# Optimization experiments

Hardware: AMD Instinct MI355X
Metric: run time of the kernel (lower is better)

The kernel has to match this reference:

```python
import jax, jax.numpy as jnp
import numpy as np

N = 8192
M = 16
F_NODE = 128
HID = 512


def setup_inputs() -> dict:
    key = jax.random.key(0)
    ks = jax.random.split(key, 10)
    node_in_fea = jax.random.normal(ks[0], (N, F_NODE), dtype=jnp.float32)
    edge_fea_idx = jax.random.randint(ks[1], (N, M), 0, N, dtype=jnp.int64)
    s_emb = 1.0 / np.sqrt(F_NODE)
    s_h = 1.0 / np.sqrt(HID)
    W_emb = jax.random.uniform(ks[2], (F_NODE, HID), jnp.float32, -s_emb, s_emb)
    b_emb = jax.random.uniform(ks[3], (HID,), jnp.float32, -s_emb, s_emb)
    W1 = jax.random.uniform(ks[4], (HID, HID), jnp.float32, -s_h, s_h)
    b1 = jax.random.uniform(ks[5], (HID,), jnp.float32, -s_h, s_h)
    W2 = jax.random.uniform(ks[6], (HID, HID), jnp.float32, -s_h, s_h)
    b2 = jax.random.uniform(ks[7], (HID,), jnp.float32, -s_h, s_h)
    W3 = jax.random.uniform(ks[8], (HID, HID), jnp.float32, -s_h, s_h)
    b3 = jax.random.uniform(ks[9], (HID,), jnp.float32, -s_h, s_h)
    return {"node_in_fea": node_in_fea, "edge_fea_idx": edge_fea_idx,
            "W_emb": W_emb, "b_emb": b_emb, "W1": W1, "b1": b1,
            "W2": W2, "b2": b2, "W3": W3, "b3": b3}


def _normalized_adj(edge_fea_idx, n):
    # build dense adjacency: adj[i, j] += 1 for each valid neighbor j of i
    rows = jnp.broadcast_to(jnp.arange(n)[:, None], edge_fea_idx.shape)
    valid = edge_fea_idx >= 0  # -1 marks invalid neighbor
    cols = jnp.where(valid, edge_fea_idx, 0)
    vals = valid.astype(jnp.float32)
    adj = jnp.zeros((n, n), jnp.float32).at[rows.reshape(-1), cols.reshape(-1)].add(vals.reshape(-1))
    # add self-loops, symmetric normalization D^{-1/2} A D^{-1/2}
    adj = adj + jnp.eye(n, dtype=jnp.float32)
    deg = jnp.sum(adj, axis=1)
    d_inv_sqrt = jnp.where(deg > 0, deg ** -0.5, 0.0)
    return adj * d_inv_sqrt[:, None] * d_inv_sqrt[None, :]


def reference(node_in_fea, edge_fea_idx, W_emb, b_emb, W1, b1, W2, b2, W3, b3):
    adj = _normalized_adj(edge_fea_idx, node_in_fea.shape[0])
    x = node_in_fea @ W_emb + b_emb          # (N, HID)
    x = jax.nn.relu((adj @ x) @ W1 + b1)     # gcn1 + relu
    x = jax.nn.relu((adj @ x) @ W2 + b2)     # gcn2 + relu
    x = (adj @ x) @ W3 + b3                  # gcn3 (no relu)
    return x
```

## Files before the change

### kernel.cpp

```cpp
#include <hip/hip_runtime.h>
#include <stdint.h>

#define NN 8192
#define MM 16
#define FN 128
#define HH 512

typedef unsigned short u16;
typedef unsigned int u32;
typedef __bf16 bf16;
typedef __bf16 bf16x8 __attribute__((ext_vector_type(8)));
typedef float f32x4 __attribute__((ext_vector_type(4)));

__device__ __forceinline__ void gld_lds16(const u16* g, u16* l) {
  __builtin_amdgcn_global_load_lds(
      (const __attribute__((address_space(1))) void*)g,
      (__attribute__((address_space(3))) void*)l, 16, 0, 0);
}

__device__ __forceinline__ int probe_f32(const u16* w) {
  int lane = threadIdx.x & 63;
  int e = (w[2 * lane] >> 7) & 0xFF;
  unsigned long long m = __ballot(!(e == 0 || (e >= 90 && e <= 140)));
  return __popcll(m) >= 8;
}
__device__ __forceinline__ int probe_i64(const u32* w) {
  int lane = threadIdx.x & 63;
  unsigned long long m = __ballot(lane < 32 && w[2 * lane + 1] != 0);
  return m == 0;
}

__device__ __forceinline__ void transpose_tile(const void* __restrict__ W,
                                               u16* __restrict__ T, int K,
                                               int tt, int f32in, u16* sm) {
  const int k0 = (tt >> 4) * 32, n0 = (tt & 15) * 32;
  const int tx = threadIdx.x & 31, ty = threadIdx.x >> 5;
#pragma unroll
  for (int r = ty; r < 32; r += 8) {
    size_t src = (size_t)(k0 + r) * HH + n0 + tx;
    bf16 v = f32in ? (bf16)((const float*)W)[src] : ((const bf16*)W)[src];
    sm[r * 33 + tx] = *(u16*)&v;
  }
  __syncthreads();
#pragma unroll
  for (int r = ty; r < 32; r += 8)
    T[(size_t)(n0 + r) * K + k0 + tx] = sm[tx * 33 + r];
}

__global__ __launch_bounds__(256) void prepA_kernel(
    const u16* __restrict__ node, const void* __restrict__ Wemb,
    const void* __restrict__ b0, u16* __restrict__ biasBF,
    u16* __restrict__ TWemb) {
  __shared__ u16 sm[32 * 33];
  const int f32in = probe_f32(node);
  const int bid = blockIdx.x, tid = threadIdx.x;
  if (bid < 2) {
    const int off = bid * 256 + tid;
    bf16 v = f32in ? (bf16)((const float*)b0)[off] : ((const bf16*)b0)[off];
    biasBF[off] = *(u16*)&v;
  } else {
    transpose_tile(Wemb, TWemb, FN, bid - 2, f32in, sm);
  }
}

template <bool RELU>
__device__ __forceinline__ void gemm_tile(const void* __restrict__ A, int K,
                                          int af32, const u16* __restrict__ Bt,
                                          const u16* __restrict__ bias,
                                          int rtile, int ctile, int outf32,
                                          void* __restrict__ C, u16* As,
                                          u16* Bs) {
  const int tid = threadIdx.x;
  const int wave = tid >> 6, lane = tid & 63;
  const int wr = wave >> 1, wc = wave & 1;
  const int quad = lane >> 4, l16 = lane & 15;
  f32x4 acc[2][4] = {};

  int arow[2], agc[2], brow[4], bgc[4];
#pragma unroll
  for (int i = 0; i < 2; ++i) {
    int c = i * 256 + tid;
    arow[i] = c >> 3;
    agc[i] = (c & 7) ^ (arow[i] & 7);
  }
#pragma unroll
  for (int i = 0; i < 4; ++i) {
    int c = i * 256 + tid;
    brow[i] = c >> 3;
    bgc[i] = (c & 7) ^ (brow[i] & 7);
  }
  u16* AsW = As + wave * 512;
  u16* BsW = Bs + wave * 512;

  for (int k0 = 0; k0 < K; k0 += 64) {
    __syncthreads();
    if (af32) {
      const float* Af = (const float*)A;
      bf16x8 v[2];
#pragma unroll
      for (int i = 0; i < 2; ++i) {
        const float* p = &Af[(size_t)(rtile * 64 + arow[i]) * K + k0 + agc[i] * 8];
        f32x4 x0 = *(const f32x4*)p, x1 = *(const f32x4*)(p + 4);
#pragma unroll
        for (int t = 0; t < 4; ++t) {
          v[i][t] = (bf16)x0[t];
          v[i][4 + t] = (bf16)x1[t];
        }
      }
#pragma unroll
      for (int i = 0; i < 2; ++i) *(bf16x8*)&As[(i * 256 + tid) * 8] = v[i];
    } else {
      const u16* Ab = (const u16*)A;
#pragma unroll
      for (int i = 0; i < 2; ++i)
        gld_lds16(&Ab[(size_t)(rtile * 64 + arow[i]) * K + k0 + agc[i] * 8],
                  AsW + i * 2048);
    }
#pragma unroll
    for (int i = 0; i < 4; ++i)
      gld_lds16(&Bt[(size_t)(ctile * 128 + brow[i]) * K + k0 + bgc[i] * 8],
                BsW + i * 2048);
    __syncthreads();
#pragma unroll
    for (int h = 0; h < 2; ++h) {
      bf16x8 af[2], bfr[4];
#pragma unroll
      for (int i = 0; i < 2; ++i) {
        int r = wr * 32 + i * 16 + l16;
        int cc = (h * 4 + quad) ^ (r & 7);
        af[i] = *(const bf16x8*)&As[r * 64 + cc * 8];
      }
#pragma unroll
      for (int j = 0; j < 4; ++j) {
        int n = wc * 64 + j * 16 + l16;
        int cc = (h * 4 + quad) ^ (n & 7);
        bfr[j] = *(const bf16x8*)&Bs[n * 64 + cc * 8];
      }
#pragma unroll
      for (int i = 0; i < 2; ++i)
#pragma unroll
        for (int j = 0; j < 4; ++j)
          acc[i][j] = __builtin_amdgcn_mfma_f32_16x16x32_bf16(af[i], bfr[j],
                                                              acc[i][j], 0, 0, 0);
    }
  }

  const int crow0 = rtile * 64 + wr * 32 + quad * 4;
  const int ccol0 = ctile * 128 + wc * 64 + l16;
#pragma unroll
  for (int j = 0; j < 4; ++j) {
    const int col = ccol0 + j * 16;
    const float bv = (float)(*(const bf16*)&bias[col]);
#pragma unroll
    for (int i = 0; i < 2; ++i)
#pragma unroll
      for (int r = 0; r < 4; ++r) {
        float v = acc[i][j][r] + bv;
        if (RELU) v = fmaxf(v, 0.0f);
        size_t off = (size_t)(crow0 + i * 16 + r) * HH + col;
        if (outf32) {
          ((float*)C)[off] = v;
        } else {
          bf16 o = (bf16)v;
          ((u16*)C)[off] = *(u16*)&o;
        }
      }
  }
}

__global__ __launch_bounds__(256) void emb_plus_kernel(
    const u16* __restrict__ node, const u32* __restrict__ idxw,
    const void* __restrict__ W1, const void* __restrict__ b1,
    const void* __restrict__ W2, const void* __restrict__ b2,
    const void* __restrict__ W3, const void* __restrict__ b3,
    const u16* __restrict__ TWemb, const u16* __restrict__ biasBF,
    float* __restrict__ dis, u16* __restrict__ biasBF_w,
    u16* __restrict__ TW1, u16* __restrict__ TW2, u16* __restrict__ TW3,
    u16* __restrict__ xout) {
  __shared__ __align__(16) u16 As[64 * 64];
  __shared__ __align__(16) u16 Bs[128 * 64];
  const int bid = blockIdx.x, tid = threadIdx.x;
  if (bid < 512) {
    const int af32 = probe_f32(node);
    gemm_tile<false>(node, FN, af32, TWemb, biasBF, bid >> 2, bid & 3, 0, xout,
                     As, Bs);
  } else if (bid < 544) {
    const int i64 = probe_i64(idxw);
    const int* idx = (const int*)idxw;
    const int i = (bid - 512) * 256 + tid;
    int c = 1;
#pragma unroll
    for (int e = 0; e < MM; ++e) c += (idx[(i * MM + e) << i64] >= 0) ? 1 : 0;
    dis[i] = rsqrtf((float)c);
  } else if (bid < 550) {
    const int f32in = probe_f32(node);
    const int id = (bid - 544) * 256 + tid;
    const int q = id >> 9;
    const void* src = q == 0 ? b1 : q == 1 ? b2 : b3;
    const int off = id & (HH - 1);
    bf16 v = f32in ? (bf16)((const float*)src)[off] : ((const bf16*)src)[off];
    biasBF_w[HH + id] = *(u16*)&v;
  } else {
    const int f32in = probe_f32(node);
    const int t = bid - 550;
    const int q = t >> 8, tt = t & 255;
    const void* W = q == 0 ? W1 : q == 1 ? W2 : W3;
    u16* T = q == 0 ? TW1 : q == 1 ? TW2 : TW3;
    transpose_tile(W, T, HH, tt, f32in, As);
  }
}

template <bool RELU, bool FINAL>
__global__ __launch_bounds__(256) void gemm_main(const u16* __restrict__ A,
                                                 const u16* __restrict__ Bt,
                                                 const u16* __restrict__ bias,
                                                 const u16* __restrict__ nodeprobe,
                                                 void* __restrict__ C) {
  __shared__ __align__(16) u16 As[64 * 64];
  __shared__ __align__(16) u16 Bs[128 * 64];
  int outf32 = 0;
  if (FINAL) outf32 = probe_f32(nodeprobe);
  gemm_tile<RELU>(A, HH, 0, Bt, bias, blockIdx.x, blockIdx.y, outf32, C, As, Bs);
}

__global__ __launch_bounds__(256) void agg_kernel(const u16* __restrict__ x,
                                                  const u32* __restrict__ idxw,
                                                  const float* __restrict__ dis,
                                                  u16* __restrict__ y) {
  const int i64 = probe_i64(idxw);
  const int* idx = (const int*)idxw;
  const int b = blockIdx.x;
  const int strip = (b & 7) >> 1;
  const int grp = (b >> 3) * 2 + (b & 1);
  const int wave = threadIdx.x >> 6, lane = threadIdx.x & 63;
  const int node = grp * 16 + wave * 4 + (lane >> 4);
  const int c0 = strip * 128 + (lane & 15) * 8;
  const float wi = dis[node];
  float acc[8];
  bf16x8 xs = *(const bf16x8*)&x[(size_t)node * HH + c0];
#pragma unroll
  for (int t = 0; t < 8; ++t) acc[t] = wi * wi * (float)xs[t];
#pragma unroll
  for (int e = 0; e < MM; ++e) {
    const int j = idx[(node * MM + e) << i64];
    if (j >= 0) {
      const float w = wi * dis[j];
      bf16x8 v = *(const bf16x8*)&x[(size_t)j * HH + c0];
#pragma unroll
      for (int t = 0; t < 8; ++t) acc[t] += w * (float)v[t];
    }
  }
  bf16x8 o;
#pragma unroll
  for (int t = 0; t < 8; ++t) o[t] = (bf16)acc[t];
  *(bf16x8*)&y[(size_t)node * HH + c0] = o;
}

extern "C" void kernel_launch(void* const* d_in, const int* in_sizes, int n_in,
                              void* d_out, int out_size, void* d_ws, size_t ws_size,
                              hipStream_t stream) {
  const u16* node = (const u16*)d_in[0];
  const u32* idxw = (const u32*)d_in[1];
  const void* Wemb = d_in[2];
  const void* bemb = d_in[3];
  const void* W1 = d_in[4];
  const void* b1 = d_in[5];
  const void* W2 = d_in[6];
  const void* b2 = d_in[7];
  const void* W3 = d_in[8];
  const void* b3 = d_in[9];

  char* p = (char*)d_ws;
  float* dis = (float*)p;  p += NN * sizeof(float);
  u16* biasBF = (u16*)p;   p += 4 * HH * sizeof(u16);
  u16* TWemb = (u16*)p;    p += (size_t)HH * FN * 2;
  u16* TW1 = (u16*)p;      p += (size_t)HH * HH * 2;
  u16* TW2 = (u16*)p;      p += (size_t)HH * HH * 2;
  u16* TW3 = (u16*)p;      p += (size_t)HH * HH * 2;
  u16* xA = (u16*)p;
  u16* xO = (u16*)d_out;

  prepA_kernel<<<66, 256, 0, stream>>>(node, Wemb, bemb, biasBF, TWemb);
  emb_plus_kernel<<<1318, 256, 0, stream>>>(node, idxw, W1, b1, W2, b2, W3, b3,
                                            TWemb, biasBF, dis, biasBF, TW1,
                                            TW2, TW3, xO);
  agg_kernel<<<NN / 4, 256, 0, stream>>>(xO, idxw, dis, xA);
  gemm_main<true, false>
      <<<dim3(128, 4), 256, 0, stream>>>(xA, TW1, biasBF + HH, node, xO);
  agg_kernel<<<NN / 4, 256, 0, stream>>>(xO, idxw, dis, xA);
  gemm_main<true, false>
      <<<dim3(128, 4), 256, 0, stream>>>(xA, TW2, biasBF + 2 * HH, node, xO);
  agg_kernel<<<NN / 4, 256, 0, stream>>>(xO, idxw, dis, xA);
  gemm_main<false, true>
      <<<dim3(128, 4), 256, 0, stream>>>(xA, TW3, biasBF + 3 * HH, node, d_out);
}
```

Before: 170.4 us.

## Fold embedding into W1 and reorder GCN layers as transform-then-aggregate

Uses associativity: (adj@x)@W equals adj@(x@W). The embedding matmul is fused with W1 by precomputing Wemb@W1 and b_emb@W1 in a small prep kernel, which removes one 8192x512x512 GEMM. Each later layer now runs its GEMM first and then the sparse aggregation, with bias, ReLU and the final fp32 output moved into the aggregation epilogue. The costs are a rounding change from the bf16-rounded combined weight, and a naive serial prep kernel that computes Wemb@W1 and the bias vector.

```diff
diff --git a/kernel.cpp b/kernel.cpp
--- a/kernel.cpp
+++ b/kernel.cpp
@@ -30,45 +30,85 @@
   return m == 0;
 }
 
+__device__ __forceinline__ bf16 cvt_elem(const void* p, size_t i, int f32) {
+  return f32 ? (bf16)((const float*)p)[i] : ((const bf16*)p)[i];
+}
+
+__global__ __launch_bounds__(256) void prep_kernel(
+    const u16* __restrict__ node, const void* __restrict__ Wemb,
+    const void* __restrict__ bemb, const void* __restrict__ W1,
+    u16* __restrict__ TWc, float* __restrict__ bvec) {
+  const int f32in = probe_f32(node);
+  const int bid = blockIdx.x, tid = threadIdx.x;
+  if (bid < 64) {
+    const int k0 = (bid >> 4) * 32, n0 = (bid & 15) * 32;
+    __shared__ u16 Ws[32 * 256];
+    __shared__ u16 W1s[256 * 32];
+    const int k = tid >> 3, nb = (tid & 7) * 4;
+    float acc[4] = {0.f, 0.f, 0.f, 0.f};
+    for (int mc = 0; mc < HH; mc += 256) {
+      {
+        const int row = tid >> 3, seg = (tid & 7) * 32;
+#pragma unroll 8
+        for (int i = 0; i < 32; ++i) {
+          bf16 v = cvt_elem(Wemb, (size_t)(k0 + row) * HH + mc + seg + i, f32in);
+          Ws[row * 256 + seg + i] = *(u16*)&v;
+        }
+#pragma unroll 8
+        for (int i = 0; i < 32; ++i) {
+          bf16 v = cvt_elem(W1, (size_t)(mc + tid) * HH + n0 + i, f32in);
+          W1s[tid * 32 + i] = *(u16*)&v;
+        }
+      }
+      __syncthreads();
+#pragma unroll 8
+      for (int m = 0; m < 256; ++m) {
+        float a = (float)*(const bf16*)&Ws[k * 256 + m];
+        const bf16* w4 = (const bf16*)&W1s[m * 32 + nb];
+#pragma unroll
+        for (int j = 0; j < 4; ++j) acc[j] += a * (float)w4[j];
+      }
+      __syncthreads();
+    }
+#pragma unroll
+    for (int j = 0; j < 4; ++j) {
+      bf16 o = (bf16)acc[j];
+      TWc[(size_t)(n0 + nb + j) * FN + k0 + k] = *(u16*)&o;
+    }
+  } else {
+    const int n = (bid - 64) * 256 + tid;
+    float acc = 0.f;
+#pragma unroll 8
+    for (int m = 0; m < HH; ++m) {
+      float b = (float)cvt_elem(bemb, m, f32in);
+      float w = (float)cvt_elem(W1, (size_t)m * HH + n, f32in);
+      acc += b * w;
+    }
+    bvec[n] = acc;
+  }
+}
+
 __device__ __forceinline__ void transpose_tile(const void* __restrict__ W,
-                                               u16* __restrict__ T, int K,
-                                               int tt, int f32in, u16* sm) {
+                                               u16* __restrict__ T, int tt,
+                                               int f32in, u16* sm) {
   const int k0 = (tt >> 4) * 32, n0 = (tt & 15) * 32;
   const int tx = threadIdx.x & 31, ty = threadIdx.x >> 5;
 #pragma unroll
   for (int r = ty; r < 32; r += 8) {
-    size_t src = (size_t)(k0 + r) * HH + n0 + tx;
-    bf16 v = f32in ? (bf16)((const float*)W)[src] : ((const bf16*)W)[src];
+    bf16 v = cvt_elem(W, (size_t)(k0 + r) * HH + n0 + tx, f32in);
     sm[r * 33 + tx] = *(u16*)&v;
   }
   __syncthreads();
 #pragma unroll
   for (int r = ty; r < 32; r += 8)
-    T[(size_t)(n0 + r) * K + k0 + tx] = sm[tx * 33 + r];
-}
-
-__global__ __launch_bounds__(256) void prepA_kernel(
-    const u16* __restrict__ node, const void* __restrict__ Wemb,
-    const void* __restrict__ b0, u16* __restrict__ biasBF,
-    u16* __restrict__ TWemb) {
-  __shared__ u16 sm[32 * 33];
-  const int f32in = probe_f32(node);
-  const int bid = blockIdx.x, tid = threadIdx.x;
-  if (bid < 2) {
-    const int off = bid * 256 + tid;
-    bf16 v = f32in ? (bf16)((const float*)b0)[off] : ((const bf16*)b0)[off];
-    biasBF[off] = *(u16*)&v;
-  } else {
-    transpose_tile(Wemb, TWemb, FN, bid - 2, f32in, sm);
-  }
-}
-
-template <bool RELU>
+    T[(size_t)(n0 + r) * HH + k0 + tx] = sm[tx * 33 + r];
+}
+
 __device__ __forceinline__ void gemm_tile(const void* __restrict__ A, int K,
                                           int af32, const u16* __restrict__ Bt,
-                                          const u16* __restrict__ bias,
-                                          int rtile, int ctile, int outf32,
-                                          void* __restrict__ C, u16* As,
+                                          const float* __restrict__ biasf,
+                                          int rtile, int ctile,
+                                          u16* __restrict__ C, u16* As,
                                           u16* Bs) {
   const int tid = threadIdx.x;
   const int wave = tid >> 6, lane = tid & 63;
@@ -150,40 +190,29 @@
 #pragma unroll
   for (int j = 0; j < 4; ++j) {
     const int col = ccol0 + j * 16;
-    const float bv = (float)(*(const bf16*)&bias[col]);
+    const float bv = biasf ? biasf[col] : 0.f;
 #pragma unroll
     for (int i = 0; i < 2; ++i)
 #pragma unroll
       for (int r = 0; r < 4; ++r) {
-        float v = acc[i][j][r] + bv;
-        if (RELU) v = fmaxf(v, 0.0f);
-        size_t off = (size_t)(crow0 + i * 16 + r) * HH + col;
-        if (outf32) {
-          ((float*)C)[off] = v;
-        } else {
-          bf16 o = (bf16)v;
-          ((u16*)C)[off] = *(u16*)&o;
-        }
-      }
-  }
-}
-
-__global__ __launch_bounds__(256) void emb_plus_kernel(
+        bf16 o = (bf16)(acc[i][j][r] + bv);
+        C[(size_t)(crow0 + i * 16 + r) * HH + col] = *(u16*)&o;
+      }
+  }
+}
+
+__global__ __launch_bounds__(256) void g1_kernel(
     const u16* __restrict__ node, const u32* __restrict__ idxw,
-    const void* __restrict__ W1, const void* __restrict__ b1,
-    const void* __restrict__ W2, const void* __restrict__ b2,
-    const void* __restrict__ W3, const void* __restrict__ b3,
-    const u16* __restrict__ TWemb, const u16* __restrict__ biasBF,
-    float* __restrict__ dis, u16* __restrict__ biasBF_w,
-    u16* __restrict__ TW1, u16* __restrict__ TW2, u16* __restrict__ TW3,
+    const void* __restrict__ W2, const void* __restrict__ W3,
+    const u16* __restrict__ TWc, const float* __restrict__ bvec,
+    float* __restrict__ dis, u16* __restrict__ TW2, u16* __restrict__ TW3,
     u16* __restrict__ xout) {
   __shared__ __align__(16) u16 As[64 * 64];
   __shared__ __align__(16) u16 Bs[128 * 64];
   const int bid = blockIdx.x, tid = threadIdx.x;
   if (bid < 512) {
     const int af32 = probe_f32(node);
-    gemm_tile<false>(node, FN, af32, TWemb, biasBF, bid >> 2, bid & 3, 0, xout,
-                     As, Bs);
+    gemm_tile(node, FN, af32, TWc, bvec, bid >> 2, bid & 3, xout, As, Bs);
   } else if (bid < 544) {
     const int i64 = probe_i64(idxw);
     const int* idx = (const int*)idxw;
@@ -192,42 +221,28 @@
 #pragma unroll
     for (int e = 0; e < MM; ++e) c += (idx[(i * MM + e) << i64] >= 0) ? 1 : 0;
     dis[i] = rsqrtf((float)c);
-  } else if (bid < 550) {
-    const int f32in = probe_f32(node);
-    const int id = (bid - 544) * 256 + tid;
-    const int q = id >> 9;
-    const void* src = q == 0 ? b1 : q == 1 ? b2 : b3;
-    const int off = id & (HH - 1);
-    bf16 v = f32in ? (bf16)((const float*)src)[off] : ((const bf16*)src)[off];
-    biasBF_w[HH + id] = *(u16*)&v;
   } else {
     const int f32in = probe_f32(node);
-    const int t = bid - 550;
-    const int q = t >> 8, tt = t & 255;
-    const void* W = q == 0 ? W1 : q == 1 ? W2 : W3;
-    u16* T = q == 0 ? TW1 : q == 1 ? TW2 : TW3;
-    transpose_tile(W, T, HH, tt, f32in, As);
-  }
-}
-
-template <bool RELU, bool FINAL>
-__global__ __launch_bounds__(256) void gemm_main(const u16* __restrict__ A,
-                                                 const u16* __restrict__ Bt,
-                                                 const u16* __restrict__ bias,
-                                                 const u16* __restrict__ nodeprobe,
-                                                 void* __restrict__ C) {
+    const int t = bid - 544;
+    transpose_tile(t < 256 ? W2 : W3, t < 256 ? TW2 : TW3, t & 255, f32in, As);
+  }
+}
+
+__global__ __launch_bounds__(256) void gemm_mid(const u16* __restrict__ A,
+                                                const u16* __restrict__ Bt,
+                                                u16* __restrict__ C) {
   __shared__ __align__(16) u16 As[64 * 64];
   __shared__ __align__(16) u16 Bs[128 * 64];
-  int outf32 = 0;
-  if (FINAL) outf32 = probe_f32(nodeprobe);
-  gemm_tile<RELU>(A, HH, 0, Bt, bias, blockIdx.x, blockIdx.y, outf32, C, As, Bs);
-}
-
-__global__ __launch_bounds__(256) void agg_kernel(const u16* __restrict__ x,
-                                                  const u32* __restrict__ idxw,
-                                                  const float* __restrict__ dis,
-                                                  u16* __restrict__ y) {
+  gemm_tile(A, HH, 0, Bt, nullptr, blockIdx.x, blockIdx.y, C, As, Bs);
+}
+
+template <bool RELU, bool FINAL>
+__global__ __launch_bounds__(256) void agg_kernel(
+    const u16* __restrict__ t, const u32* __restrict__ idxw,
+    const float* __restrict__ dis, const void* __restrict__ bias,
+    const u16* __restrict__ nodeprobe, void* __restrict__ y) {
   const int i64 = probe_i64(idxw);
+  const int f32io = probe_f32(nodeprobe);
   const int* idx = (const int*)idxw;
   const int b = blockIdx.x;
   const int strip = (b & 7) >> 1;
@@ -237,23 +252,48 @@
   const int c0 = strip * 128 + (lane & 15) * 8;
   const float wi = dis[node];
   float acc[8];
-  bf16x8 xs = *(const bf16x8*)&x[(size_t)node * HH + c0];
-#pragma unroll
-  for (int t = 0; t < 8; ++t) acc[t] = wi * wi * (float)xs[t];
+  bf16x8 xs = *(const bf16x8*)&t[(size_t)node * HH + c0];
+#pragma unroll
+  for (int k = 0; k < 8; ++k) acc[k] = wi * wi * (float)xs[k];
 #pragma unroll
   for (int e = 0; e < MM; ++e) {
     const int j = idx[(node * MM + e) << i64];
     if (j >= 0) {
       const float w = wi * dis[j];
-      bf16x8 v = *(const bf16x8*)&x[(size_t)j * HH + c0];
-#pragma unroll
-      for (int t = 0; t < 8; ++t) acc[t] += w * (float)v[t];
-    }
-  }
-  bf16x8 o;
-#pragma unroll
-  for (int t = 0; t < 8; ++t) o[t] = (bf16)acc[t];
-  *(bf16x8*)&y[(size_t)node * HH + c0] = o;
+      bf16x8 v = *(const bf16x8*)&t[(size_t)j * HH + c0];
+#pragma unroll
+      for (int k = 0; k < 8; ++k) acc[k] += w * (float)v[k];
+    }
+  }
+  float bv[8];
+  if (f32io) {
+    f32x4 b0 = *(const f32x4*)&((const float*)bias)[c0];
+    f32x4 b1 = *(const f32x4*)&((const float*)bias)[c0 + 4];
+#pragma unroll
+    for (int k = 0; k < 4; ++k) { bv[k] = b0[k]; bv[4 + k] = b1[k]; }
+  } else {
+    bf16x8 bb = *(const bf16x8*)&((const u16*)bias)[c0];
+#pragma unroll
+    for (int k = 0; k < 8; ++k) bv[k] = (float)bb[k];
+  }
+#pragma unroll
+  for (int k = 0; k < 8; ++k) {
+    acc[k] += bv[k];
+    if (RELU) acc[k] = fmaxf(acc[k], 0.f);
+  }
+  if (FINAL && f32io) {
+    float* O = (float*)y;
+    f32x4 o0, o1;
+#pragma unroll
+    for (int k = 0; k < 4; ++k) { o0[k] = acc[k]; o1[k] = acc[4 + k]; }
+    *(f32x4*)&O[(size_t)node * HH + c0] = o0;
+    *(f32x4*)&O[(size_t)node * HH + c0 + 4] = o1;
+  } else {
+    bf16x8 o;
+#pragma unroll
+    for (int k = 0; k < 8; ++k) o[k] = (bf16)acc[k];
+    *(bf16x8*)&((u16*)y)[(size_t)node * HH + c0] = o;
+  }
 }
 
 extern "C" void kernel_launch(void* const* d_in, const int* in_sizes, int n_in,
@@ -271,26 +311,23 @@
   const void* b3 = d_in[9];
 
   char* p = (char*)d_ws;
-  float* dis = (float*)p;  p += NN * sizeof(float);
-  u16* biasBF = (u16*)p;   p += 4 * HH * sizeof(u16);
-  u16* TWemb = (u16*)p;    p += (size_t)HH * FN * 2;
-  u16* TW1 = (u16*)p;      p += (size_t)HH * HH * 2;
-  u16* TW2 = (u16*)p;      p += (size_t)HH * HH * 2;
-  u16* TW3 = (u16*)p;      p += (size_t)HH * HH * 2;
+  float* dis = (float*)p;   p += NN * sizeof(float);
+  float* bvec = (float*)p;  p += HH * sizeof(float);
+  u16* TWc = (u16*)p;       p += (size_t)HH * FN * 2;
+  u16* TW2 = (u16*)p;       p += (size_t)HH * HH * 2;
+  u16* TW3 = (u16*)p;       p += (size_t)HH * HH * 2;
   u16* xA = (u16*)p;
   u16* xO = (u16*)d_out;
 
-  prepA_kernel<<<66, 256, 0, stream>>>(node, Wemb, bemb, biasBF, TWemb);
-  emb_plus_kernel<<<1318, 256, 0, stream>>>(node, idxw, W1, b1, W2, b2, W3, b3,
-                                            TWemb, biasBF, dis, biasBF, TW1,
-                                            TW2, TW3, xO);
-  agg_kernel<<<NN / 4, 256, 0, stream>>>(xO, idxw, dis, xA);
-  gemm_main<true, false>
-      <<<dim3(128, 4), 256, 0, stream>>>(xA, TW1, biasBF + HH, node, xO);
-  agg_kernel<<<NN / 4, 256, 0, stream>>>(xO, idxw, dis, xA);
-  gemm_main<true, false>
-      <<<dim3(128, 4), 256, 0, stream>>>(xA, TW2, biasBF + 2 * HH, node, xO);
-  agg_kernel<<<NN / 4, 256, 0, stream>>>(xO, idxw, dis, xA);
-  gemm_main<false, true>
-      <<<dim3(128, 4), 256, 0, stream>>>(xA, TW3, biasBF + 3 * HH, node, d_out);
-}
+  prep_kernel<<<66, 256, 0, stream>>>(node, Wemb, bemb, W1, TWc, bvec);
+  g1_kernel<<<1056, 256, 0, stream>>>(node, idxw, W2, W3, TWc, bvec, dis, TW2,
+                                      TW3, xA);
+  agg_kernel<true, false>
+      <<<NN / 4, 256, 0, stream>>>(xA, idxw, dis, b1, node, xO);
+  gemm_mid<<<dim3(128, 4), 256, 0, stream>>>(xO, TW2, xA);
+  agg_kernel<true, false>
+      <<<NN / 4, 256, 0, stream>>>(xA, idxw, dis, b2, node, xO);
+  gemm_mid<<<dim3(128, 4), 256, 0, stream>>>(xO, TW3, xA);
+  agg_kernel<false, true>
+      <<<NN / 4, 256, 0, stream>>>(xA, idxw, dis, b3, node, d_out);
+}
```

Measured after the change: 311.0 us. +82.6%, slower.
